# Kernel tuning notes

Measured on AMD Instinct MI355X. Metric: run time of the kernel, lower is better.

The kernel has to match this reference:

```python
import jax, jax.numpy as jnp
import numpy as np

TOPK = 8
NOISE_EPS = 0.01
_SQRT2 = np.sqrt(2.0).astype(np.float32)

def _norm_cdf(v):
    return 0.5 * (1.0 + jax.lax.erf(v / _SQRT2))

def setup_inputs() -> dict:
    key = jax.random.key(0)
    k1, k2, k3, k4 = jax.random.split(key, 4)
    B, D, E = 16384, 4096, 64
    return {
        "x": jax.random.normal(k1, (B, D), dtype=jnp.float32),
        "w_gate": jax.random.normal(k2, (D, E), dtype=jnp.float32) * 0.02,
        "w_noise": jax.random.normal(k3, (D, E), dtype=jnp.float32) * 0.02,
        "noise": jax.random.normal(k4, (B, E), dtype=jnp.float32),
    }

def reference(x, w_gate, w_noise, noise):
    B = x.shape[0]
    clean_logits = x @ w_gate                                   # [B, E]
    noise_stddev = jax.nn.softplus(x @ w_noise) + NOISE_EPS      # [B, E]
    noisy_logits = clean_logits + noise * noise_stddev           # [B, E]
    # NOTE: original applies softmax BEFORE topk (probabilities, not logits)
    probs = jax.nn.softmax(noisy_logits, axis=1)                 # [B, E]
    top_logits, top_indices = jax.lax.top_k(probs, TOPK + 1)     # [B, k+1]
    top_k_gates = jax.nn.softmax(top_logits[:, :TOPK], axis=1)   # [B, k]
    rows = jnp.arange(B)[:, None]
    gates = jnp.zeros_like(probs).at[rows, top_indices[:, :TOPK]].set(top_k_gates)
    # _prob_in_top_k: thresholds are the (topk)-th and (topk-1)-th top probs
    thr_in = top_logits[:, TOPK:TOPK + 1]                        # [B, 1]
    thr_out = top_logits[:, TOPK - 1:TOPK]                       # [B, 1]
    is_in = noisy_logits > thr_in                                # (faithful: raw noisy vs prob threshold)
    prob_if_in = _norm_cdf((clean_logits - thr_in) / noise_stddev)
    prob_if_out = _norm_cdf((clean_logits - thr_out) / noise_stddev)
    load = jnp.where(is_in, prob_if_in, prob_if_out).sum(axis=0)  # [E]
    return gates, load
```

## Files before the change

### kernel.cpp

```cpp
#include <hip/hip_runtime.h>
#include <math.h>

#define BB 16384
#define DD 4096
#define EE 64
#define TK 8
#define RT 32

typedef __attribute__((ext_vector_type(8))) short s16x8;
typedef __attribute__((ext_vector_type(4))) float f32x4;

__device__ inline unsigned pack_hi2(float a, float b) {
    return (__float_as_uint(a) >> 16) | (__float_as_uint(b) & 0xFFFF0000u);
}
__device__ inline float hi_part(float a) {
    return __uint_as_float(__float_as_uint(a) & 0xFFFF0000u);
}
__device__ inline void split_pack(const float4& v0, const float4& v1, uint4& h, uint4& l) {
    h.x = pack_hi2(v0.x, v0.y); h.y = pack_hi2(v0.z, v0.w);
    h.z = pack_hi2(v1.x, v1.y); h.w = pack_hi2(v1.z, v1.w);
    l.x = pack_hi2(v0.x - hi_part(v0.x), v0.y - hi_part(v0.y));
    l.y = pack_hi2(v0.z - hi_part(v0.z), v0.w - hi_part(v0.w));
    l.z = pack_hi2(v1.x - hi_part(v1.x), v1.y - hi_part(v1.y));
    l.w = pack_hi2(v1.z - hi_part(v1.z), v1.w - hi_part(v1.w));
}

__global__ __launch_bounds__(256, 1)
void prep_w(const float* __restrict__ wg, const float* __restrict__ wn,
            char* __restrict__ wsB)
{
    __shared__ float Wtmp[64 * 132];
    const int t  = threadIdx.x;
    const int kc = blockIdx.x;

#pragma unroll
    for (int i = 0; i < 8; ++i) {
        int fid = t + i * 256;
        int m   = fid >> 10;
        int id  = fid & 1023;
        int kk  = id >> 4;
        int n4  = id & 15;
        const float* src = (m ? wn : wg) + (size_t)(kc * 64 + kk) * EE + n4 * 4;
        float4 v = *(const float4*)src;
        *(float4*)&Wtmp[kk * 132 + m * 64 + n4 * 4] = v;
    }
    __syncthreads();

#pragma unroll
    for (int i = 0; i < 4; ++i) {
        int id  = t + i * 256;
        int sub = id >> 9;
        int nt  = (id >> 6) & 7;
        int ln  = id & 63;
        int n   = nt * 16 + (ln & 15);
        int k0  = sub * 32 + (ln >> 4) * 8;
        float f[8];
#pragma unroll
        for (int j = 0; j < 8; ++j) f[j] = Wtmp[(k0 + j) * 132 + n];
        uint4 h, l;
        h.x = pack_hi2(f[0], f[1]); h.y = pack_hi2(f[2], f[3]);
        h.z = pack_hi2(f[4], f[5]); h.w = pack_hi2(f[6], f[7]);
        l.x = pack_hi2(f[0] - hi_part(f[0]), f[1] - hi_part(f[1]));
        l.y = pack_hi2(f[2] - hi_part(f[2]), f[3] - hi_part(f[3]));
        l.z = pack_hi2(f[4] - hi_part(f[4]), f[5] - hi_part(f[5]));
        l.w = pack_hi2(f[6] - hi_part(f[6]), f[7] - hi_part(f[7]));
        size_t base = (size_t)kc * 32768;
        *(uint4*)(wsB + base + (size_t)(((sub * 2 + 0) * 8 + nt) * 64 + ln) * 16) = h;
        *(uint4*)(wsB + base + (size_t)(((sub * 2 + 1) * 8 + nt) * 64 + ln) * 16) = l;
    }
}

__global__ __launch_bounds__(256, 1)
void moe_mfma(const float* __restrict__ x,
              const float* __restrict__ noise,
              const char* __restrict__ wsB,
              float* __restrict__ gates,
              float* __restrict__ load)
{
    __shared__ uint4 Bbuf[2][2048];
    __shared__ float red[256];

    const int tid  = threadIdx.x;
    const int w    = tid >> 6;
    const int lane = tid & 63;
    const int wm   = w >> 1;
    const int wnh  = w & 1;
    const int rb   = blockIdx.x * RT;

    const int m16 = lane & 15;
    const int q   = lane >> 4;

    const float* xbase = x + (size_t)(rb + wm * 16 + m16) * DD + q * 8;

    f32x4 acc[4];
#pragma unroll
    for (int nt = 0; nt < 4; ++nt) acc[nt] = (f32x4){0.f, 0.f, 0.f, 0.f};

    auto issue_dma = [&](int ch, int b) {
        const char* gB = wsB + (size_t)ch * 32768;
#pragma unroll
        for (int i = 0; i < 8; ++i) {
            const int si = w * 8 + i;
            __builtin_amdgcn_global_load_lds(
                (const __attribute__((address_space(1))) unsigned int*)(gB + (size_t)si * 1024 + lane * 16),
                (__attribute__((address_space(3))) unsigned int*)&Bbuf[b][si * 64],
                16, 0, 0);
        }
    };
    auto load_a = [&](int ch, float4* xv) {
#pragma unroll
        for (int sub = 0; sub < 2; ++sub) {
            const float* p = xbase + ch * 64 + sub * 32;
            xv[sub * 2 + 0] = *(const float4*)p;
            xv[sub * 2 + 1] = *(const float4*)(p + 4);
        }
    };
    auto compute = [&](int b, const float4* xv) {
#pragma unroll
        for (int sub = 0; sub < 2; ++sub) {
            uint4 h, l;
            split_pack(xv[sub * 2 + 0], xv[sub * 2 + 1], h, l);
            const s16x8 ah = __builtin_bit_cast(s16x8, h);
            const s16x8 al = __builtin_bit_cast(s16x8, l);
#pragma unroll
            for (int nt = 0; nt < 4; ++nt) {
                const s16x8 bh = *(const s16x8*)&Bbuf[b][((sub * 2 + 0) * 8 + wnh * 4 + nt) * 64 + lane];
                const s16x8 bl = *(const s16x8*)&Bbuf[b][((sub * 2 + 1) * 8 + wnh * 4 + nt) * 64 + lane];
                acc[nt] = __builtin_amdgcn_mfma_f32_16x16x32_bf16(ah, bh, acc[nt], 0, 0, 0);
                acc[nt] = __builtin_amdgcn_mfma_f32_16x16x32_bf16(ah, bl, acc[nt], 0, 0, 0);
                acc[nt] = __builtin_amdgcn_mfma_f32_16x16x32_bf16(al, bh, acc[nt], 0, 0, 0);
            }
        }
    };

    float4 xva[4], xvb[4];
    issue_dma(0, 0);
    load_a(0, xva);

    for (int ch = 0; ch < 64; ch += 2) {
        __syncthreads();
        issue_dma(ch + 1, 1);
        load_a(ch + 1, xvb);
        compute(0, xva);
        __syncthreads();
        if (ch + 2 < 64) {
            issue_dma(ch + 2, 0);
            load_a(ch + 2, xva);
        }
        compute(1, xvb);
    }

    __syncthreads();
    float* Ls = (float*)&Bbuf[0][0];
    const int q4 = lane >> 4, cc = lane & 15;
#pragma unroll
    for (int nt = 0; nt < 4; ++nt)
#pragma unroll
        for (int r = 0; r < 4; ++r)
            Ls[(wm * 16 + q4 * 4 + r) * 132 + wnh * 64 + nt * 16 + cc] = acc[nt][r];
    __syncthreads();

    float loadAcc = 0.f;
    for (int rr = 0; rr < 8; ++rr) {
        const int row = w * 8 + rr;
        const float clean = Ls[row * 132 + lane];
        const float rawn  = Ls[row * 132 + 64 + lane];
        const float nz    = noise[(size_t)(rb + row) * EE + lane];

        const float sp = fmaxf(rawn, 0.f) + log1pf(expf(-fabsf(rawn)));
        const float sd = sp + 0.01f;
        const float noisy = clean + nz * sd;

        float m = noisy;
#pragma unroll
        for (int off = 32; off; off >>= 1) m = fmaxf(m, __shfl_xor(m, off));
        const float ex = expf(noisy - m);
        float s = ex;
#pragma unroll
        for (int off = 32; off; off >>= 1) s += __shfl_xor(s, off);
        const float p = ex / s;

        float cur = p;
        int selrank = -1;
        float v[9];
#pragma unroll
        for (int j = 0; j < 9; ++j) {
            float bv = cur;
            int   bi = lane;
#pragma unroll
            for (int off = 32; off; off >>= 1) {
                const float ov = __shfl_xor(bv, off);
                const int   oi = __shfl_xor(bi, off);
                if (ov > bv || (ov == bv && oi < bi)) { bv = ov; bi = oi; }
            }
            v[j] = bv;
            if (lane == bi) { cur = -1.f; if (j < TK) selrank = j; }
        }

        float denom = 0.f;
#pragma unroll
        for (int j = 0; j < TK; ++j) denom += expf(v[j] - v[0]);
        const float gate = (selrank >= 0) ? (expf(p - v[0]) / denom) : 0.f;
        gates[(size_t)(rb + row) * EE + lane] = gate;

        const float thr_in  = v[8];
        const float thr_out = v[7];
        const bool  is_in   = noisy > thr_in;
        const float a = (clean - (is_in ? thr_in : thr_out)) / sd;
        loadAcc += 0.5f * (1.f + erff(a * 0.70710678118654752f));
    }

    red[w * 64 + lane] = loadAcc;
    __syncthreads();
    if (tid < 64) {
        const float s = red[tid] + red[64 + tid] + red[128 + tid] + red[192 + tid];
        atomicAdd(&load[tid], s);
    }
}

extern "C" void kernel_launch(void* const* d_in, const int* in_sizes, int n_in,
                              void* d_out, int out_size, void* d_ws, size_t ws_size,
                              hipStream_t stream)
{
    const float* x     = (const float*)d_in[0];
    const float* wg    = (const float*)d_in[1];
    const float* wn    = (const float*)d_in[2];
    const float* noise = (const float*)d_in[3];
    float* gates = (float*)d_out;
    float* load  = (float*)d_out + (size_t)BB * EE;
    char*  wsB   = (char*)d_ws;

    hipMemsetAsync(load, 0, EE * sizeof(float), stream);
    hipLaunchKernelGGL(prep_w, dim3(DD / 64), dim3(256), 0, stream, wg, wn, wsB);
    hipLaunchKernelGGL(moe_mfma, dim3(BB / RT), dim3(256), 0, stream,
                       x, noise, wsB, gates, load);
}
```

Measured before the change: 500.1 us.

## Stage x tiles through LDS via async DMA and re-tile warps over N

The x activations now go through LDS with global_load_lds DMA instead of register loads. The K chunk drops from 64 to 32 and the double-buffer iteration count doubles. Each warp now covers both 16-row M tiles and a 32-column slice of N, so every A fragment feeds more MFMAs while each B fragment is shared. Launch bounds rise to 2 blocks per CU and the smaller LDS footprint supports this, with the aim of better latency hiding. In exchange the kernel runs twice as many barriers per K pass, and the sched barriers constrain instruction scheduling.

```diff
diff --git a/kernel.cpp b/kernel.cpp
--- a/kernel.cpp
+++ b/kernel.cpp
@@ -70,94 +70,105 @@
     }
 }
 
-__global__ __launch_bounds__(256, 1)
+__global__ __launch_bounds__(256, 2)
 void moe_mfma(const float* __restrict__ x,
               const float* __restrict__ noise,
               const char* __restrict__ wsB,
               float* __restrict__ gates,
               float* __restrict__ load)
 {
-    __shared__ uint4 Bbuf[2][2048];
+    __shared__ char  smem[2 * 4096 + 2 * 16384];
     __shared__ float red[256];
+    char* const Ab0 = smem;
+    char* const Ab1 = smem + 4096;
+    char* const Bb0 = smem + 8192;
+    char* const Bb1 = smem + 8192 + 16384;
 
     const int tid  = threadIdx.x;
     const int w    = tid >> 6;
     const int lane = tid & 63;
-    const int wm   = w >> 1;
-    const int wnh  = w & 1;
     const int rb   = blockIdx.x * RT;
 
-    const int m16 = lane & 15;
-    const int q   = lane >> 4;
-
-    const float* xbase = x + (size_t)(rb + wm * 16 + m16) * DD + q * 8;
-
-    f32x4 acc[4];
-#pragma unroll
-    for (int nt = 0; nt < 4; ++nt) acc[nt] = (f32x4){0.f, 0.f, 0.f, 0.f};
-
-    auto issue_dma = [&](int ch, int b) {
-        const char* gB = wsB + (size_t)ch * 32768;
-#pragma unroll
-        for (int i = 0; i < 8; ++i) {
-            const int si = w * 8 + i;
+    const int mt_s = tid >> 7;
+    const int q_s  = (tid >> 5) & 3;
+    const int h_s  = (tid >> 4) & 1;
+    const int m_s  = tid & 15;
+    const float* xa = x + (size_t)(rb + mt_s * 16 + m_s) * DD + q_s * 8 + h_s * 4;
+    const int aslot = (tid >> 6) * 1024;
+
+    f32x4 acc[2][2];
+#pragma unroll
+    for (int mt = 0; mt < 2; ++mt)
+#pragma unroll
+        for (int nt = 0; nt < 2; ++nt) acc[mt][nt] = (f32x4){0.f, 0.f, 0.f, 0.f};
+
+    auto issueA = [&](int ch, char* Ab) {
+        __builtin_amdgcn_global_load_lds(
+            (const __attribute__((address_space(1))) unsigned int*)(xa + ch * 32),
+            (__attribute__((address_space(3))) unsigned int*)(Ab + aslot),
+            16, 0, 0);
+    };
+    auto issueB = [&](int ch, char* Bb) {
+        const char* gB = wsB + (size_t)(ch >> 1) * 32768 + (size_t)(ch & 1) * 16384;
+#pragma unroll
+        for (int i = 0; i < 4; ++i) {
+            const int si = w * 4 + i;
             __builtin_amdgcn_global_load_lds(
                 (const __attribute__((address_space(1))) unsigned int*)(gB + (size_t)si * 1024 + lane * 16),
-                (__attribute__((address_space(3))) unsigned int*)&Bbuf[b][si * 64],
+                (__attribute__((address_space(3))) unsigned int*)(Bb + si * 1024),
                 16, 0, 0);
         }
     };
-    auto load_a = [&](int ch, float4* xv) {
-#pragma unroll
-        for (int sub = 0; sub < 2; ++sub) {
-            const float* p = xbase + ch * 64 + sub * 32;
-            xv[sub * 2 + 0] = *(const float4*)p;
-            xv[sub * 2 + 1] = *(const float4*)(p + 4);
-        }
-    };
-    auto compute = [&](int b, const float4* xv) {
-#pragma unroll
-        for (int sub = 0; sub < 2; ++sub) {
+    auto compute = [&](const char* Ab, const char* Bb) {
+        const int q = lane >> 4, m16 = lane & 15;
+#pragma unroll
+        for (int mt = 0; mt < 2; ++mt) {
+            const char* ab = Ab + (mt * 128 + q * 32 + m16) * 16;
+            const float4 v0 = *(const float4*)ab;
+            const float4 v1 = *(const float4*)(ab + 256);
             uint4 h, l;
-            split_pack(xv[sub * 2 + 0], xv[sub * 2 + 1], h, l);
+            split_pack(v0, v1, h, l);
             const s16x8 ah = __builtin_bit_cast(s16x8, h);
             const s16x8 al = __builtin_bit_cast(s16x8, l);
 #pragma unroll
-            for (int nt = 0; nt < 4; ++nt) {
-                const s16x8 bh = *(const s16x8*)&Bbuf[b][((sub * 2 + 0) * 8 + wnh * 4 + nt) * 64 + lane];
-                const s16x8 bl = *(const s16x8*)&Bbuf[b][((sub * 2 + 1) * 8 + wnh * 4 + nt) * 64 + lane];
-                acc[nt] = __builtin_amdgcn_mfma_f32_16x16x32_bf16(ah, bh, acc[nt], 0, 0, 0);
-                acc[nt] = __builtin_amdgcn_mfma_f32_16x16x32_bf16(ah, bl, acc[nt], 0, 0, 0);
-                acc[nt] = __builtin_amdgcn_mfma_f32_16x16x32_bf16(al, bh, acc[nt], 0, 0, 0);
+            for (int nt = 0; nt < 2; ++nt) {
+                const s16x8 bh = *(const s16x8*)(Bb + (((0 * 8) + w * 2 + nt) * 64 + lane) * 16);
+                const s16x8 bl = *(const s16x8*)(Bb + (((1 * 8) + w * 2 + nt) * 64 + lane) * 16);
+                acc[mt][nt] = __builtin_amdgcn_mfma_f32_16x16x32_bf16(ah, bh, acc[mt][nt], 0, 0, 0);
+                acc[mt][nt] = __builtin_amdgcn_mfma_f32_16x16x32_bf16(ah, bl, acc[mt][nt], 0, 0, 0);
+                acc[mt][nt] = __builtin_amdgcn_mfma_f32_16x16x32_bf16(al, bh, acc[mt][nt], 0, 0, 0);
             }
         }
     };
 
-    float4 xva[4], xvb[4];
-    issue_dma(0, 0);
-    load_a(0, xva);
-
-    for (int ch = 0; ch < 64; ch += 2) {
+    issueA(0, Ab0);
+    issueB(0, Bb0);
+
+    for (int ch = 0; ch < 128; ch += 2) {
         __syncthreads();
-        issue_dma(ch + 1, 1);
-        load_a(ch + 1, xvb);
-        compute(0, xva);
+        issueA(ch + 1, Ab1);
+        issueB(ch + 1, Bb1);
+        __builtin_amdgcn_sched_barrier(0);
+        compute(Ab0, Bb0);
         __syncthreads();
-        if (ch + 2 < 64) {
-            issue_dma(ch + 2, 0);
-            load_a(ch + 2, xva);
-        }
-        compute(1, xvb);
-    }
-
-    __syncthreads();
-    float* Ls = (float*)&Bbuf[0][0];
+        if (ch + 2 < 128) {
+            issueA(ch + 2, Ab0);
+            issueB(ch + 2, Bb0);
+        }
+        __builtin_amdgcn_sched_barrier(0);
+        compute(Ab1, Bb1);
+    }
+
+    __syncthreads();
+    float* Ls = (float*)smem;
     const int q4 = lane >> 4, cc = lane & 15;
 #pragma unroll
-    for (int nt = 0; nt < 4; ++nt)
-#pragma unroll
-        for (int r = 0; r < 4; ++r)
-            Ls[(wm * 16 + q4 * 4 + r) * 132 + wnh * 64 + nt * 16 + cc] = acc[nt][r];
+    for (int mt = 0; mt < 2; ++mt)
+#pragma unroll
+        for (int nt = 0; nt < 2; ++nt)
+#pragma unroll
+            for (int r = 0; r < 4; ++r)
+                Ls[(mt * 16 + q4 * 4 + r) * 132 + w * 32 + nt * 16 + cc] = acc[mt][nt][r];
     __syncthreads();
 
     float loadAcc = 0.f;
```

Measured after the change: 492.4 us. Within noise of the previous version (-1.5%).
